# Kernel optimization log

Hardware: AMD Instinct MI355X
Metric: run time of the kernel (lower is better)

## Reference

```python
import jax, jax.numpy as jnp
import numpy as np

B, C, P, H, W, S = 4, 256, 128, 56, 56, 5
EPS = 1e-5


def setup_inputs() -> dict:
    key = jax.random.key(0)
    ks = jax.random.split(key, 6)
    return {
        "x": jax.random.normal(ks[0], (B, C, H, W), jnp.float32),
        "Wt": jax.random.normal(ks[1], (P, C), jnp.float32) * 0.05,
        "Wp": jax.random.normal(ks[2], (P, C), jnp.float32) * 0.05,
        "Wg": jax.random.normal(ks[3], (S, P, C), jnp.float32) * 0.05,
        "W1": jax.random.normal(ks[4], (S, C, P), jnp.float32) * 0.05,
        "W2": jax.random.normal(ks[5], (S, C, P), jnp.float32) * 0.05,
        "gamma": jnp.ones((S, C), jnp.float32),
        "beta": jnp.zeros((S, C), jnp.float32),
    }


def _batchnorm(o, g, b):
    # training-mode BN over (batch, spatial); o: [b, C, n]
    mean = o.mean(axis=(0, 2), keepdims=True)
    var = ((o - mean) ** 2).mean(axis=(0, 2), keepdims=True)
    return (o - mean) * jax.lax.rsqrt(var + EPS) * g[None, :, None] + b[None, :, None]


def reference(x, Wt, Wp, Wg, W1, W2, gamma, beta):
    b, c, h, w = x.shape
    n = h * w
    xf = x.reshape(b, c, n)
    # 1x1 conv projections == channel matmuls
    t = jax.nn.relu(jnp.einsum('pc,bcn->bpn', Wt, xf))  # is_norm branch uses relu
    p = jax.nn.relu(jnp.einsum('pc,bcn->bpn', Wp, xf))
    att = jnp.einsum('bpi,bpj->bij', t, p)              # [b, n, n] affinity
    att = 0.5 * (att + jnp.swapaxes(att, 1, 2))         # is_sys symmetrization
    d = att.sum(axis=2)                                  # degree [b, n]
    d_safe = jnp.where(d != 0, d, 1.0)
    d_inv = jnp.where(d != 0, jax.lax.rsqrt(d_safe), 0.0)
    att = att * d_inv[:, None, :] * d_inv[:, :, None]    # D^-1/2 A D^-1/2
    out = xf
    for s in range(S):  # fixed small stage count
        g = jnp.einsum('pc,bcn->bpn', Wg[s], out)        # [b, P, n]
        ag = jnp.einsum('bij,bpj->bpi', att, g)          # att @ g over spatial
        o = jnp.einsum('cp,bpn->bcn', W1[s], ag) + jnp.einsum('cp,bpn->bcn', W2[s], g)
        out = _batchnorm(o, gamma[s], beta[s]) + out     # BN + residual
    return out.reshape(b, c, h, w)
```

## Files before the change

### kernel.cpp

```cpp
#include <hip/hip_runtime.h>

namespace {

constexpr int Bc = 4;
constexpr int Cc = 256;
constexpr int Pc = 128;
constexpr int Nc = 3136;
constexpr int Sc = 5;
constexpr int KSn = 7;
constexpr int KCH = 448;
constexpr float EPSc = 1e-5f;

typedef __attribute__((ext_vector_type(8))) short bf16x8;
typedef __attribute__((ext_vector_type(4))) float f32x4;
typedef __attribute__((ext_vector_type(8))) unsigned short u16x8;
typedef __attribute__((ext_vector_type(4))) unsigned short u16x4;

__device__ inline float bf2f(unsigned short u) {
    return __uint_as_float(((unsigned)u) << 16);
}
__device__ inline unsigned short f2bf(float f) {
    unsigned u = __float_as_uint(f);
    return (unsigned short)((u + 0x7FFFu + ((u >> 16) & 1u)) >> 16);
}

template <int EPI, bool DUAL, int CMOUT, bool SPLITK, int BNSTAT, bool F32OUT>
__global__ __launch_bounds__(256) void mgemm(
    const unsigned short* __restrict__ A, int lda, long aB,
    const unsigned short* __restrict__ Bw, int ldb, long bB,
    const unsigned short* __restrict__ A2, const unsigned short* __restrict__ B2,
    unsigned short* __restrict__ outSM, int ldsm, long smB, long smSlice,
    unsigned short* __restrict__ outCM, long cmB,
    float* __restrict__ ps, float* __restrict__ ps2,
    int K, int kchunk, const float* __restrict__ dinv)
{
    constexpr int TB = 64 * 64 * 2;
    constexpr int NT = DUAL ? 4 : 2;
    __shared__ __align__(16) char lds[2 * NT * TB];

    int b, kstart, kend;
    long smOff;
    if (SPLITK) {
        b = blockIdx.z & 3;
        int ks = blockIdx.z >> 2;
        kstart = ks * kchunk;
        kend = kstart + kchunk;
        smOff = (long)ks * smSlice;
    } else {
        b = blockIdx.z; kstart = 0; kend = K; smOff = 0;
    }
    const int n0 = blockIdx.x * 64;
    const int m0 = blockIdx.y * 64;
    const int tid = threadIdx.x;
    const int w = tid >> 6, l = tid & 63;

    const unsigned short* Ab  = A + (size_t)b * aB + (size_t)m0 * lda;
    const unsigned short* A2b = DUAL ? (A2 + (size_t)b * aB + (size_t)m0 * lda) : nullptr;
    const unsigned short* Bb  = Bw + (size_t)b * bB + (size_t)n0 * ldb;
    const unsigned short* B2b = DUAL ? (B2 + (size_t)b * bB + (size_t)n0 * ldb) : nullptr;

    const int srow = w * 16 + (l >> 3);
    const int gsw = ((l & 7) ^ (l >> 3)) * 8;
    const size_t aO0 = (size_t)srow * lda + gsw;
    const size_t aO1 = aO0 + (size_t)8 * lda;
    const size_t bO0 = (size_t)srow * ldb + gsw;
    const size_t bO1 = bO0 + (size_t)8 * ldb;
    const int wch = w * 2048;

    f32x4 acc[4] = {};

    auto stage = [&](int buf, int k0) {
        char* base = lds + buf * (NT * TB);
        __builtin_amdgcn_global_load_lds(
            (const __attribute__((address_space(1))) void*)(Ab + k0 + aO0),
            (__attribute__((address_space(3))) void*)(base + wch), 16, 0, 0);
        __builtin_amdgcn_global_load_lds(
            (const __attribute__((address_space(1))) void*)(Ab + k0 + aO1),
            (__attribute__((address_space(3))) void*)(base + wch + 1024), 16, 0, 0);
        __builtin_amdgcn_global_load_lds(
            (const __attribute__((address_space(1))) void*)(Bb + k0 + bO0),
            (__attribute__((address_space(3))) void*)(base + TB + wch), 16, 0, 0);
        __builtin_amdgcn_global_load_lds(
            (const __attribute__((address_space(1))) void*)(Bb + k0 + bO1),
            (__attribute__((address_space(3))) void*)(base + TB + wch + 1024), 16, 0, 0);
        if (DUAL) {
            __builtin_amdgcn_global_load_lds(
                (const __attribute__((address_space(1))) void*)(A2b + k0 + aO0),
                (__attribute__((address_space(3))) void*)(base + 2 * TB + wch), 16, 0, 0);
            __builtin_amdgcn_global_load_lds(
                (const __attribute__((address_space(1))) void*)(A2b + k0 + aO1),
                (__attribute__((address_space(3))) void*)(base + 2 * TB + wch + 1024), 16, 0, 0);
            __builtin_amdgcn_global_load_lds(
                (const __attribute__((address_space(1))) void*)(B2b + k0 + bO0),
                (__attribute__((address_space(3))) void*)(base + 3 * TB + wch), 16, 0, 0);
            __builtin_amdgcn_global_load_lds(
                (const __attribute__((address_space(1))) void*)(B2b + k0 + bO1),
                (__attribute__((address_space(3))) void*)(base + 3 * TB + wch + 1024), 16, 0, 0);
        }
    };

    auto compute = [&](int buf) {
        const char* base = lds + buf * (NT * TB);
        const int lo = l & 15, gq = l >> 4;
        const int brow = w * 16 + lo;
#pragma unroll
        for (int kh = 0; kh < 2; ++kh) {
            const int lg = kh * 4 + gq;
            bf16x8 bf = *(const bf16x8*)(base + TB + brow * 128 + ((lg ^ (brow & 7)) << 4));
#pragma unroll
            for (int r = 0; r < 4; ++r) {
                int row = r * 16 + lo;
                bf16x8 af = *(const bf16x8*)(base + row * 128 + ((lg ^ (row & 7)) << 4));
                acc[r] = __builtin_amdgcn_mfma_f32_16x16x32_bf16(af, bf, acc[r], 0, 0, 0);
            }
            if (DUAL) {
                bf16x8 bf2 = *(const bf16x8*)(base + 3 * TB + brow * 128 + ((lg ^ (brow & 7)) << 4));
#pragma unroll
                for (int r = 0; r < 4; ++r) {
                    int row = r * 16 + lo;
                    bf16x8 a2 = *(const bf16x8*)(base + 2 * TB + row * 128 + ((lg ^ (row & 7)) << 4));
                    acc[r] = __builtin_amdgcn_mfma_f32_16x16x32_bf16(a2, bf2, acc[r], 0, 0, 0);
                }
            }
        }
    };

    stage(0, kstart);
    __syncthreads();
    const int nst = (kend - kstart) >> 6;
    for (int s = 0; s < nst; ++s) {
        if (s + 1 < nst) stage((s + 1) & 1, kstart + ((s + 1) << 6));
        compute(s & 1);
        __syncthreads();
    }

    float* ot = (float*)lds;
#pragma unroll
    for (int r = 0; r < 4; ++r) {
#pragma unroll
        for (int j = 0; j < 4; ++j) {
            float v = acc[r][j];
            if (EPI == 1) v = fmaxf(v, 0.f);
            ot[(r * 16 + (l >> 4) * 4 + j) * 65 + (w * 16 + (l & 15))] = v;
        }
    }
    __syncthreads();

    if (F32OUT) {
        const int r = tid >> 2, c0 = (tid & 3) * 16;
        float* dst = (float*)outSM + (size_t)b * smB + smOff +
                     (size_t)(m0 + r) * ldsm + n0 + c0;
#pragma unroll
        for (int k = 0; k < 4; ++k) {
            float4 v;
            v.x = ot[r * 65 + c0 + 4 * k + 0];
            v.y = ot[r * 65 + c0 + 4 * k + 1];
            v.z = ot[r * 65 + c0 + 4 * k + 2];
            v.w = ot[r * 65 + c0 + 4 * k + 3];
            *(float4*)(dst + 4 * k) = v;
        }
    } else {
        const int r = tid >> 2, c0 = (tid & 3) * 16;
        float sc = 1.f;
        if (EPI == 2) sc = 0.5f * dinv[(size_t)b * Nc + m0 + r];
        u16x8 o1, o2;
#pragma unroll
        for (int j = 0; j < 8; ++j) {
            float v = ot[r * 65 + c0 + j];
            if (EPI == 2) v *= sc;
            o1[j] = f2bf(v);
        }
#pragma unroll
        for (int j = 0; j < 8; ++j) {
            float v = ot[r * 65 + c0 + 8 + j];
            if (EPI == 2) v *= sc;
            o2[j] = f2bf(v);
        }
        unsigned short* dst = outSM + (size_t)b * smB + smOff +
                              (size_t)(m0 + r) * ldsm + n0 + c0;
        *(u16x8*)dst = o1;
        *(u16x8*)(dst + 8) = o2;
    }

    if (CMOUT) {
        const int c = tid >> 2, r0 = (tid & 3) * 16;
        const float* dv = dinv + (size_t)b * Nc + m0 + r0;
        u16x8 o1, o2;
#pragma unroll
        for (int j = 0; j < 8; ++j) {
            float v = ot[(r0 + j) * 65 + c];
            if (CMOUT == 2) v *= dv[j];
            o1[j] = f2bf(v);
        }
#pragma unroll
        for (int j = 0; j < 8; ++j) {
            float v = ot[(r0 + 8 + j) * 65 + c];
            if (CMOUT == 2) v *= dv[8 + j];
            o2[j] = f2bf(v);
        }
        unsigned short* dst = outCM + (size_t)b * cmB + (size_t)(n0 + c) * Nc + m0 + r0;
        *(u16x8*)dst = o1;
        *(u16x8*)(dst + 8) = o2;
    }

    if (BNSTAT) {
        float* p1 = (float*)(lds + 16896);
        float* p2 = p1 + 256;
        const int col = tid & 63, rq = tid >> 6;
        float s = 0.f, s2 = 0.f;
#pragma unroll
        for (int i = 0; i < 16; ++i) {
            float v = ot[(rq * 16 + i) * 65 + col];
            s += v;
            if (BNSTAT == 2) s2 = fmaf(v, v, s2);
        }
        p1[rq * 64 + col] = s;
        if (BNSTAT == 2) p2[rq * 64 + col] = s2;
        __syncthreads();
        if (tid < 64) {
            float a = 0.f, a2 = 0.f;
#pragma unroll
            for (int q = 0; q < 4; ++q) {
                a += p1[q * 64 + tid];
                if (BNSTAT == 2) a2 += p2[q * 64 + tid];
            }
            size_t slot = ((size_t)b * 49 + blockIdx.y) * 256 + n0 + tid;
            ps[slot] = a;
            if (BNSTAT == 2) ps2[slot] = a2;
        }
    }
}

__global__ __launch_bounds__(256) void cvtw_k(
    const float* __restrict__ Wt, const float* __restrict__ Wp,
    const float* __restrict__ Wg, const float* __restrict__ W1,
    const float* __restrict__ W2,
    unsigned short* __restrict__ Wcomb, unsigned short* __restrict__ Wgh,
    unsigned short* __restrict__ W1h, unsigned short* __restrict__ W2h)
{
    size_t e = ((size_t)blockIdx.x * 256 + threadIdx.x) * 4;
    const float* src; unsigned short* dst;
    if (e < 32768)            { src = Wt + e;                    dst = Wcomb + e; }
    else if (e < 65536)       { src = Wp + (e - 32768);          dst = Wcomb + e; }
    else if (e < 65536 + 163840)     { size_t o = e - 65536;          src = Wg + o; dst = Wgh + o; }
    else if (e < 65536 + 2 * 163840) { size_t o = e - 65536 - 163840; src = W1 + o; dst = W1h + o; }
    else                             { size_t o = e - 65536 - 327680; src = W2 + o; dst = W2h + o; }
    float4 v = *(const float4*)src;
    u16x4 t;
    t[0] = f2bf(v.x); t[1] = f2bf(v.y); t[2] = f2bf(v.z); t[3] = f2bf(v.w);
    *(u16x4*)dst = t;
}

__global__ __launch_bounds__(256) void xpin_k(
    const float* __restrict__ x, float* __restrict__ out_sm,
    unsigned short* __restrict__ outh)
{
    __shared__ float tb[64][65];
    int b = blockIdx.z, c0 = blockIdx.y * 64, n0 = blockIdx.x * 64;
    int t = threadIdx.x;
    {
        int ci = t >> 2, nb = (t & 3) * 16;
        const float* src = x + ((size_t)b * Cc + c0 + ci) * Nc + n0 + nb;
#pragma unroll
        for (int k = 0; k < 4; ++k) {
            float4 v = *(const float4*)(src + 4 * k);
            tb[ci][nb + 4 * k + 0] = v.x; tb[ci][nb + 4 * k + 1] = v.y;
            tb[ci][nb + 4 * k + 2] = v.z; tb[ci][nb + 4 * k + 3] = v.w;
        }
    }
    __syncthreads();
    {
        int r = t >> 2, cb = (t & 3) * 16;
        size_t off = ((size_t)b * Nc + n0 + r) * Cc + c0 + cb;
        float vv[16];
#pragma unroll
        for (int j = 0; j < 16; ++j) vv[j] = tb[cb + j][r];
        float* dst = out_sm + off;
#pragma unroll
        for (int k = 0; k < 4; ++k) {
            float4 v; v.x = vv[4*k]; v.y = vv[4*k+1]; v.z = vv[4*k+2]; v.w = vv[4*k+3];
            *(float4*)(dst + 4 * k) = v;
        }
        u16x8 h1, h2;
#pragma unroll
        for (int j = 0; j < 8; ++j) { h1[j] = f2bf(vv[j]); h2[j] = f2bf(vv[8 + j]); }
        unsigned short* dh = outh + off;
        *(u16x8*)dh = h1;
        *(u16x8*)(dh + 8) = h2;
    }
}

__global__ __launch_bounds__(256) void xpout_k(
    const float* __restrict__ out_sm, float* __restrict__ outp)
{
    __shared__ float tb[64][65];
    int b = blockIdx.z, c0 = blockIdx.y * 64, n0 = blockIdx.x * 64;
    int t = threadIdx.x;
    {
        int r = t >> 2, cb = (t & 3) * 16;
        const float* src = out_sm + ((size_t)b * Nc + n0 + r) * Cc + c0 + cb;
#pragma unroll
        for (int k = 0; k < 4; ++k) {
            float4 v = *(const float4*)(src + 4 * k);
            tb[r][cb + 4 * k + 0] = v.x; tb[r][cb + 4 * k + 1] = v.y;
            tb[r][cb + 4 * k + 2] = v.z; tb[r][cb + 4 * k + 3] = v.w;
        }
    }
    __syncthreads();
    {
        int c = t >> 2, rb = (t & 3) * 16;
        float vv[16];
#pragma unroll
        for (int j = 0; j < 16; ++j) vv[j] = tb[rb + j][c];
        float* dst = outp + ((size_t)b * Cc + c0 + c) * Nc + n0 + rb;
#pragma unroll
        for (int k = 0; k < 4; ++k) {
            float4 v; v.x = vv[4*k]; v.y = vv[4*k+1]; v.z = vv[4*k+2]; v.w = vv[4*k+3];
            *(float4*)(dst + 4 * k) = v;
        }
    }
}

__global__ __launch_bounds__(256) void dinv_k(
    const unsigned short* __restrict__ U, const float* __restrict__ rp,
    float* __restrict__ dinv)
{
    __shared__ float rsl[256];
    int b = blockIdx.y, tid = threadIdx.x;
    float s = 0.f;
    for (int j = 0; j < 49; ++j) s += rp[((size_t)b * 49 + j) * 256 + tid];
    rsl[tid ^ 128] = s;
    __syncthreads();
    int i = blockIdx.x * 256 + tid;
    if (i < Nc) {
        const unsigned short* row = U + ((size_t)b * Nc + i) * 256;
        float acc = 0.f;
        for (int q0 = 0; q0 < 256; q0 += 8) {
            u16x8 v = *(const u16x8*)(row + q0);
#pragma unroll
            for (int j = 0; j < 8; ++j) acc = fmaf(bf2f(v[j]), rsl[q0 + j], acc);
        }
        float d = 0.5f * acc;
        dinv[(size_t)b * Nc + i] = d > 0.f ? rsqrtf(d) : 0.f;
    }
}

__global__ __launch_bounds__(256) void redmst_k(
    const float* __restrict__ Cpart, unsigned short* __restrict__ MstT)
{
    int e8 = blockIdx.x * 256 + threadIdx.x;
    int bp = e8 >> 5, qc = e8 & 31;
    size_t dstOff = ((size_t)bp * 32 + qc) * 8;
    size_t srcOff = ((size_t)bp * 32 + (qc ^ 16)) * 8;
    float4 s0 = {0.f, 0.f, 0.f, 0.f}, s1 = {0.f, 0.f, 0.f, 0.f};
    for (int ks = 0; ks < KSn; ++ks) {
        const float* base = Cpart + (size_t)ks * (Bc * Pc * Cc) + srcOff;
        float4 v0 = *(const float4*)base;
        float4 v1 = *(const float4*)(base + 4);
        s0.x += v0.x; s0.y += v0.y; s0.z += v0.z; s0.w += v0.w;
        s1.x += v1.x; s1.y += v1.y; s1.z += v1.z; s1.w += v1.w;
    }
    u16x8 o;
    o[0] = f2bf(s0.x); o[1] = f2bf(s0.y); o[2] = f2bf(s0.z); o[3] = f2bf(s0.w);
    o[4] = f2bf(s1.x); o[5] = f2bf(s1.y); o[6] = f2bf(s1.z); o[7] = f2bf(s1.w);
    *(u16x8*)(MstT + dstOff) = o;
}

__global__ __launch_bounds__(256) void bnfin_k(
    const float* __restrict__ ps, const float* __restrict__ ps2,
    const float* __restrict__ gamma, const float* __restrict__ beta,
    float* __restrict__ scale, float* __restrict__ shift)
{
    int c = threadIdx.x;
    float a = 0.f, a2 = 0.f;
    for (int g = 0; g < 196; ++g) {
        a += ps[(size_t)g * 256 + c];
        a2 += ps2[(size_t)g * 256 + c];
    }
    const float inv = 1.f / (float)(Bc * Nc);
    float mean = a * inv;
    float var = a2 * inv - mean * mean;
    float sc = gamma[c] * rsqrtf(var + EPSc);
    scale[c] = sc;
    shift[c] = beta[c] - mean * sc;
}

__global__ __launch_bounds__(256) void bnapp_k(
    const unsigned short* __restrict__ o, const float* __restrict__ scale,
    const float* __restrict__ shift, float* __restrict__ out_sm,
    unsigned short* __restrict__ outh)
{
    __shared__ float lsc[256], lsh[256];
    int t = threadIdx.x;
    lsc[t] = scale[t];
    lsh[t] = shift[t];
    __syncthreads();
    size_t e = ((size_t)blockIdx.x * 256 + t) * 8;
    int c8 = (int)(e & 255);
    u16x8 ov = *(const u16x8*)(o + e);
    float* op = out_sm + e;
    float4 o1 = *(float4*)op, o2 = *(float4*)(op + 4);
    float r[8];
#pragma unroll
    for (int j = 0; j < 8; ++j) r[j] = fmaf(bf2f(ov[j]), lsc[c8 + j], lsh[c8 + j]);
    o1.x += r[0]; o1.y += r[1]; o1.z += r[2]; o1.w += r[3];
    o2.x += r[4]; o2.y += r[5]; o2.z += r[6]; o2.w += r[7];
    *(float4*)op = o1;
    *(float4*)(op + 4) = o2;
    u16x8 hv;
    hv[0] = f2bf(o1.x); hv[1] = f2bf(o1.y); hv[2] = f2bf(o1.z); hv[3] = f2bf(o1.w);
    hv[4] = f2bf(o2.x); hv[5] = f2bf(o2.y); hv[6] = f2bf(o2.z); hv[7] = f2bf(o2.w);
    *(u16x8*)(outh + e) = hv;
}

}

extern "C" void kernel_launch(void* const* d_in, const int* in_sizes, int n_in,
                              void* d_out, int out_size, void* d_ws, size_t ws_size,
                              hipStream_t stream) {
    const float* x     = (const float*)d_in[0];
    const float* Wt    = (const float*)d_in[1];
    const float* Wp    = (const float*)d_in[2];
    const float* Wg    = (const float*)d_in[3];
    const float* W1    = (const float*)d_in[4];
    const float* W2    = (const float*)d_in[5];
    const float* gamma = (const float*)d_in[6];
    const float* beta  = (const float*)d_in[7];

    char* p = (char*)d_ws;
    auto alloc = [&](size_t bytes) { char* r = p; p += (bytes + 255) & ~(size_t)255; return r; };
    float*          out_sm = (float*)         alloc((size_t)Bc * Nc * Cc * 4);
    unsigned short* outh   = (unsigned short*)alloc((size_t)Bc * Nc * Cc * 2);
    unsigned short* U_sm   = (unsigned short*)alloc((size_t)Bc * Nc * 256 * 2);
    unsigned short* U_cm   = (unsigned short*)alloc((size_t)Bc * 256 * Nc * 2);
    unsigned short* g_sm   = (unsigned short*)alloc((size_t)Bc * Nc * Pc * 2);
    unsigned short* g_cmd  = (unsigned short*)alloc((size_t)Bc * Pc * Nc * 2);
    unsigned short* ag_sm  = (unsigned short*)alloc((size_t)Bc * Nc * Pc * 2);
    unsigned short* o_sm   = (unsigned short*)alloc((size_t)Bc * Nc * Cc * 2);
    float*          Cpart  = (float*)         alloc((size_t)KSn * Bc * Pc * Cc * 4);
    unsigned short* MstT   = (unsigned short*)alloc((size_t)Bc * Pc * Cc * 2);
    unsigned short* Wcomb  = (unsigned short*)alloc((size_t)Cc * Cc * 2);
    unsigned short* Wgh    = (unsigned short*)alloc((size_t)Sc * Pc * Cc * 2);
    unsigned short* W1h    = (unsigned short*)alloc((size_t)Sc * Cc * Pc * 2);
    unsigned short* W2h    = (unsigned short*)alloc((size_t)Sc * Cc * Pc * 2);
    float*          rp     = (float*)         alloc((size_t)Bc * 49 * 256 * 4);
    float*          dinv   = (float*)         alloc((size_t)Bc * Nc * 4);
    float*          ps     = (float*)         alloc((size_t)196 * 256 * 4);
    float*          ps2    = (float*)         alloc((size_t)196 * 256 * 4);
    float*          scale  = (float*)         alloc(256 * 4);
    float*          shiftb = (float*)         alloc(256 * 4);

    const long NC256 = (long)Nc * 256;
    const long NC128 = (long)Nc * 128;
    dim3 blk(256);

    cvtw_k<<<544, blk, 0, stream>>>(Wt, Wp, Wg, W1, W2, Wcomb, Wgh, W1h, W2h);
    xpin_k<<<dim3(49, 4, Bc), blk, 0, stream>>>(x, out_sm, outh);

    mgemm<1, false, 1, false, 1, false><<<dim3(4, 49, Bc), blk, 0, stream>>>(
        outh, 256, NC256, Wcomb, 256, 0, nullptr, nullptr,
        U_sm, 256, NC256, 0, U_cm, (long)256 * Nc, rp, nullptr, 256, 0, nullptr);

    dinv_k<<<dim3(13, Bc), blk, 0, stream>>>(U_sm, rp, dinv);

    for (int s = 0; s < Sc; ++s) {
        mgemm<0, false, 2, false, 0, false><<<dim3(2, 49, Bc), blk, 0, stream>>>(
            outh, 256, NC256, Wgh + (size_t)s * Pc * Cc, 256, 0, nullptr, nullptr,
            g_sm, 128, NC128, 0, g_cmd, (long)Pc * Nc, nullptr, nullptr, 256, 0, dinv);
        mgemm<0, false, 0, true, 0, true><<<dim3(4, 2, KSn * Bc), blk, 0, stream>>>(
            g_cmd, Nc, (long)Pc * Nc, U_cm, Nc, (long)256 * Nc, nullptr, nullptr,
            (unsigned short*)Cpart, 256, (long)Pc * Cc, (long)Bc * Pc * Cc,
            nullptr, 0, nullptr, nullptr, Nc, KCH, nullptr);
        redmst_k<<<64, blk, 0, stream>>>(Cpart, MstT);
        mgemm<2, false, 0, false, 0, false><<<dim3(2, 49, Bc), blk, 0, stream>>>(
            U_sm, 256, NC256, MstT, 256, (long)Pc * Cc, nullptr, nullptr,
            ag_sm, 128, NC128, 0, nullptr, 0, nullptr, nullptr, 256, 0, dinv);
        mgemm<0, true, 0, false, 2, false><<<dim3(4, 49, Bc), blk, 0, stream>>>(
            ag_sm, 128, NC128, W1h + (size_t)s * Cc * Pc, 128, 0,
            g_sm, W2h + (size_t)s * Cc * Pc,
            o_sm, 256, NC256, 0, nullptr, 0, ps, ps2, 128, 0, nullptr);
        bnfin_k<<<1, blk, 0, stream>>>(ps, ps2, gamma + s * Cc, beta + s * Cc,
                                       scale, shiftb);
        bnapp_k<<<1568, blk, 0, stream>>>(o_sm, scale, shiftb, out_sm, outh);
    }

    xpout_k<<<dim3(49, 4, Bc), blk, 0, stream>>>(out_sm, (float*)d_out);
}
```

Baseline: 300.7 us.

## Widen GEMM tiles to 64x128, concatenate W1/W2 into one K=256 GEMM, parallelize bnfin

The shared GEMM kernel's output tile grows from 64x64 to 64x128, with each wave computing two 16-column MFMA blocks so every A fragment feeds two MFMAs. The DUAL path is dropped: g and ag are written into one interleaved [N,256] buffer and W1/W2 are packed into a concatenated weight, so the output projection becomes a single K=256 GEMM. The BN finalize kernel now spreads across 16 blocks with an LDS reduction instead of running as a single block. The aim is more operand reuse per LDS load and less launch and serial overhead. The cost is about half as many blocks for the already small grids, which lowers occupancy and parallelism, plus a larger LDS footprint.

After: 280.0 us. -6.9%, faster.

```diff
diff --git a/kernel.cpp b/kernel.cpp
--- a/kernel.cpp
+++ b/kernel.cpp
@@ -24,19 +24,19 @@
     return (unsigned short)((u + 0x7FFFu + ((u >> 16) & 1u)) >> 16);
 }
 
-template <int EPI, bool DUAL, int CMOUT, bool SPLITK, int BNSTAT, bool F32OUT>
+template <int EPI, int CMOUT, bool SPLITK, int BNSTAT, bool F32OUT>
 __global__ __launch_bounds__(256) void mgemm(
     const unsigned short* __restrict__ A, int lda, long aB,
     const unsigned short* __restrict__ Bw, int ldb, long bB,
-    const unsigned short* __restrict__ A2, const unsigned short* __restrict__ B2,
     unsigned short* __restrict__ outSM, int ldsm, long smB, long smSlice,
     unsigned short* __restrict__ outCM, long cmB,
     float* __restrict__ ps, float* __restrict__ ps2,
     int K, int kchunk, const float* __restrict__ dinv)
 {
-    constexpr int TB = 64 * 64 * 2;
-    constexpr int NT = DUAL ? 4 : 2;
-    __shared__ __align__(16) char lds[2 * NT * TB];
+    constexpr int TBA = 64 * 64 * 2;
+    constexpr int TBB = 128 * 64 * 2;
+    constexpr int BUF = TBA + TBB;
+    __shared__ __align__(16) char lds[2 * BUF];
 
     int b, kstart, kend;
     long smOff;
@@ -49,78 +49,57 @@
     } else {
         b = blockIdx.z; kstart = 0; kend = K; smOff = 0;
     }
-    const int n0 = blockIdx.x * 64;
+    const int n0 = blockIdx.x * 128;
     const int m0 = blockIdx.y * 64;
     const int tid = threadIdx.x;
     const int w = tid >> 6, l = tid & 63;
 
-    const unsigned short* Ab  = A + (size_t)b * aB + (size_t)m0 * lda;
-    const unsigned short* A2b = DUAL ? (A2 + (size_t)b * aB + (size_t)m0 * lda) : nullptr;
-    const unsigned short* Bb  = Bw + (size_t)b * bB + (size_t)n0 * ldb;
-    const unsigned short* B2b = DUAL ? (B2 + (size_t)b * bB + (size_t)n0 * ldb) : nullptr;
-
-    const int srow = w * 16 + (l >> 3);
+    const unsigned short* Ab = A + (size_t)b * aB + (size_t)m0 * lda;
+    const unsigned short* Bb = Bw + (size_t)b * bB + (size_t)n0 * ldb;
+
+    const int srow = w * 8 + (l >> 3);
     const int gsw = ((l & 7) ^ (l >> 3)) * 8;
-    const size_t aO0 = (size_t)srow * lda + gsw;
-    const size_t aO1 = aO0 + (size_t)8 * lda;
-    const size_t bO0 = (size_t)srow * ldb + gsw;
-    const size_t bO1 = bO0 + (size_t)8 * ldb;
-    const int wch = w * 2048;
-
-    f32x4 acc[4] = {};
+
+    f32x4 acc[4][2] = {};
 
     auto stage = [&](int buf, int k0) {
-        char* base = lds + buf * (NT * TB);
-        __builtin_amdgcn_global_load_lds(
-            (const __attribute__((address_space(1))) void*)(Ab + k0 + aO0),
-            (__attribute__((address_space(3))) void*)(base + wch), 16, 0, 0);
-        __builtin_amdgcn_global_load_lds(
-            (const __attribute__((address_space(1))) void*)(Ab + k0 + aO1),
-            (__attribute__((address_space(3))) void*)(base + wch + 1024), 16, 0, 0);
-        __builtin_amdgcn_global_load_lds(
-            (const __attribute__((address_space(1))) void*)(Bb + k0 + bO0),
-            (__attribute__((address_space(3))) void*)(base + TB + wch), 16, 0, 0);
-        __builtin_amdgcn_global_load_lds(
-            (const __attribute__((address_space(1))) void*)(Bb + k0 + bO1),
-            (__attribute__((address_space(3))) void*)(base + TB + wch + 1024), 16, 0, 0);
-        if (DUAL) {
+        char* base = lds + buf * BUF;
+#pragma unroll
+        for (int j = 0; j < 2; ++j) {
             __builtin_amdgcn_global_load_lds(
-                (const __attribute__((address_space(1))) void*)(A2b + k0 + aO0),
-                (__attribute__((address_space(3))) void*)(base + 2 * TB + wch), 16, 0, 0);
+                (const __attribute__((address_space(1))) void*)
+                    (Ab + (size_t)(j * 32 + srow) * lda + k0 + gsw),
+                (__attribute__((address_space(3))) void*)(base + j * 4096 + w * 1024),
+                16, 0, 0);
+        }
+#pragma unroll
+        for (int j = 0; j < 4; ++j) {
             __builtin_amdgcn_global_load_lds(
-                (const __attribute__((address_space(1))) void*)(A2b + k0 + aO1),
-                (__attribute__((address_space(3))) void*)(base + 2 * TB + wch + 1024), 16, 0, 0);
-            __builtin_amdgcn_global_load_lds(
-                (const __attribute__((address_space(1))) void*)(B2b + k0 + bO0),
-                (__attribute__((address_space(3))) void*)(base + 3 * TB + wch), 16, 0, 0);
-            __builtin_amdgcn_global_load_lds(
-                (const __attribute__((address_space(1))) void*)(B2b + k0 + bO1),
-                (__attribute__((address_space(3))) void*)(base + 3 * TB + wch + 1024), 16, 0, 0);
+                (const __attribute__((address_space(1))) void*)
+                    (Bb + (size_t)(j * 32 + srow) * ldb + k0 + gsw),
+                (__attribute__((address_space(3))) void*)(base + TBA + j * 4096 + w * 1024),
+                16, 0, 0);
         }
     };
 
     auto compute = [&](int buf) {
-        const char* base = lds + buf * (NT * TB);
+        const char* base = lds + buf * BUF;
         const int lo = l & 15, gq = l >> 4;
-        const int brow = w * 16 + lo;
 #pragma unroll
         for (int kh = 0; kh < 2; ++kh) {
             const int lg = kh * 4 + gq;
-            bf16x8 bf = *(const bf16x8*)(base + TB + brow * 128 + ((lg ^ (brow & 7)) << 4));
+            bf16x8 bf[2];
+#pragma unroll
+            for (int c = 0; c < 2; ++c) {
+                int brow = w * 32 + c * 16 + lo;
+                bf[c] = *(const bf16x8*)(base + TBA + brow * 128 + ((lg ^ (brow & 7)) << 4));
+            }
 #pragma unroll
             for (int r = 0; r < 4; ++r) {
                 int row = r * 16 + lo;
                 bf16x8 af = *(const bf16x8*)(base + row * 128 + ((lg ^ (row & 7)) << 4));
-                acc[r] = __builtin_amdgcn_mfma_f32_16x16x32_bf16(af, bf, acc[r], 0, 0, 0);
-            }
-            if (DUAL) {
-                bf16x8 bf2 = *(const bf16x8*)(base + 3 * TB + brow * 128 + ((lg ^ (brow & 7)) << 4));
-#pragma unroll
-                for (int r = 0; r < 4; ++r) {
-                    int row = r * 16 + lo;
-                    bf16x8 a2 = *(const bf16x8*)(base + 2 * TB + row * 128 + ((lg ^ (row & 7)) << 4));
-                    acc[r] = __builtin_amdgcn_mfma_f32_16x16x32_bf16(a2, bf2, acc[r], 0, 0, 0);
-                }
+                acc[r][0] = __builtin_amdgcn_mfma_f32_16x16x32_bf16(af, bf[0], acc[r][0], 0, 0, 0);
+                acc[r][1] = __builtin_amdgcn_mfma_f32_16x16x32_bf16(af, bf[1], acc[r][1], 0, 0, 0);
             }
         }
     };
@@ -135,98 +114,90 @@
     }
 
     float* ot = (float*)lds;
-#pragma unroll
-    for (int r = 0; r < 4; ++r) {
-#pragma unroll
-        for (int j = 0; j < 4; ++j) {
-            float v = acc[r][j];
-            if (EPI == 1) v = fmaxf(v, 0.f);
-            ot[(r * 16 + (l >> 4) * 4 + j) * 65 + (w * 16 + (l & 15))] = v;
-        }
-    }
-    __syncthreads();
-
-    if (F32OUT) {
-        const int r = tid >> 2, c0 = (tid & 3) * 16;
-        float* dst = (float*)outSM + (size_t)b * smB + smOff +
-                     (size_t)(m0 + r) * ldsm + n0 + c0;
+    {
+        const int lo = l & 15, gq = l >> 4;
+#pragma unroll
+        for (int r = 0; r < 4; ++r)
+#pragma unroll
+            for (int c = 0; c < 2; ++c)
+#pragma unroll
+                for (int j = 0; j < 4; ++j) {
+                    float v = acc[r][c][j];
+                    if (EPI == 1) v = fmaxf(v, 0.f);
+                    ot[(r * 16 + gq * 4 + j) * 132 + w * 32 + c * 16 + lo] = v;
+                }
+    }
+    __syncthreads();
+
+    {
+        const int r = tid >> 2, c0 = (tid & 3) * 32;
+        if (F32OUT) {
+            float* dst = (float*)outSM + (size_t)b * smB + smOff +
+                         (size_t)(m0 + r) * ldsm + n0 + c0;
+#pragma unroll
+            for (int k = 0; k < 8; ++k) {
+                float4 v;
+                v.x = ot[r * 132 + c0 + 4 * k + 0];
+                v.y = ot[r * 132 + c0 + 4 * k + 1];
+                v.z = ot[r * 132 + c0 + 4 * k + 2];
+                v.w = ot[r * 132 + c0 + 4 * k + 3];
+                *(float4*)(dst + 4 * k) = v;
+            }
+        } else {
+            float sc = 1.f;
+            if (EPI == 2) sc = 0.5f * dinv[(size_t)b * Nc + m0 + r];
+            unsigned short* dst = outSM + (size_t)b * smB + smOff +
+                                  (size_t)(m0 + r) * ldsm + n0 + c0;
+#pragma unroll
+            for (int k = 0; k < 4; ++k) {
+                u16x8 o;
+#pragma unroll
+                for (int j = 0; j < 8; ++j) {
+                    float v = ot[r * 132 + c0 + 8 * k + j];
+                    if (EPI == 2) v *= sc;
+                    o[j] = f2bf(v);
+                }
+                *(u16x8*)(dst + 8 * k) = o;
+            }
+        }
+    }
+
+    if (CMOUT) {
+        const int c = tid >> 1, r0 = (tid & 1) * 32;
+        const float* dv = dinv + (size_t)b * Nc + m0 + r0;
+        unsigned short* dst = outCM + (size_t)b * cmB + (size_t)(n0 + c) * Nc + m0 + r0;
 #pragma unroll
         for (int k = 0; k < 4; ++k) {
-            float4 v;
-            v.x = ot[r * 65 + c0 + 4 * k + 0];
-            v.y = ot[r * 65 + c0 + 4 * k + 1];
-            v.z = ot[r * 65 + c0 + 4 * k + 2];
-            v.w = ot[r * 65 + c0 + 4 * k + 3];
-            *(float4*)(dst + 4 * k) = v;
-        }
-    } else {
-        const int r = tid >> 2, c0 = (tid & 3) * 16;
-        float sc = 1.f;
-        if (EPI == 2) sc = 0.5f * dinv[(size_t)b * Nc + m0 + r];
-        u16x8 o1, o2;
-#pragma unroll
-        for (int j = 0; j < 8; ++j) {
-            float v = ot[r * 65 + c0 + j];
-            if (EPI == 2) v *= sc;
-            o1[j] = f2bf(v);
-        }
-#pragma unroll
-        for (int j = 0; j < 8; ++j) {
-            float v = ot[r * 65 + c0 + 8 + j];
-            if (EPI == 2) v *= sc;
-            o2[j] = f2bf(v);
-        }
-        unsigned short* dst = outSM + (size_t)b * smB + smOff +
-                              (size_t)(m0 + r) * ldsm + n0 + c0;
-        *(u16x8*)dst = o1;
-        *(u16x8*)(dst + 8) = o2;
-    }
-
-    if (CMOUT) {
-        const int c = tid >> 2, r0 = (tid & 3) * 16;
-        const float* dv = dinv + (size_t)b * Nc + m0 + r0;
-        u16x8 o1, o2;
-#pragma unroll
-        for (int j = 0; j < 8; ++j) {
-            float v = ot[(r0 + j) * 65 + c];
-            if (CMOUT == 2) v *= dv[j];
-            o1[j] = f2bf(v);
-        }
-#pragma unroll
-        for (int j = 0; j < 8; ++j) {
-            float v = ot[(r0 + 8 + j) * 65 + c];
-            if (CMOUT == 2) v *= dv[8 + j];
-            o2[j] = f2bf(v);
-        }
-        unsigned short* dst = outCM + (size_t)b * cmB + (size_t)(n0 + c) * Nc + m0 + r0;
-        *(u16x8*)dst = o1;
-        *(u16x8*)(dst + 8) = o2;
+            u16x8 o;
+#pragma unroll
+            for (int j = 0; j < 8; ++j) {
+                float v = ot[(r0 + 8 * k + j) * 132 + c];
+                if (CMOUT == 2) v *= dv[8 * k + j];
+                o[j] = f2bf(v);
+            }
+            *(u16x8*)(dst + 8 * k) = o;
+        }
     }
 
     if (BNSTAT) {
-        float* p1 = (float*)(lds + 16896);
+        float* p1 = (float*)(lds + 35840);
         float* p2 = p1 + 256;
-        const int col = tid & 63, rq = tid >> 6;
+        const int col = tid & 127, half = tid >> 7;
         float s = 0.f, s2 = 0.f;
 #pragma unroll
-        for (int i = 0; i < 16; ++i) {
-            float v = ot[(rq * 16 + i) * 65 + col];
+        for (int i = 0; i < 32; ++i) {
+            float v = ot[(half * 32 + i) * 132 + col];
             s += v;
             if (BNSTAT == 2) s2 = fmaf(v, v, s2);
         }
-        p1[rq * 64 + col] = s;
-        if (BNSTAT == 2) p2[rq * 64 + col] = s2;
+        p1[half * 128 + col] = s;
+        if (BNSTAT == 2) p2[half * 128 + col] = s2;
         __syncthreads();
-        if (tid < 64) {
-            float a = 0.f, a2 = 0.f;
-#pragma unroll
-            for (int q = 0; q < 4; ++q) {
-                a += p1[q * 64 + tid];
-                if (BNSTAT == 2) a2 += p2[q * 64 + tid];
-            }
+        if (tid < 128) {
+            float a = p1[tid] + p1[128 + tid];
             size_t slot = ((size_t)b * 49 + blockIdx.y) * 256 + n0 + tid;
             ps[slot] = a;
-            if (BNSTAT == 2) ps2[slot] = a2;
+            if (BNSTAT == 2) ps2[slot] = p2[tid] + p2[128 + tid];
         }
     }
 }
@@ -236,15 +207,21 @@
     const float* __restrict__ Wg, const float* __restrict__ W1,
     const float* __restrict__ W2,
     unsigned short* __restrict__ Wcomb, unsigned short* __restrict__ Wgh,
-    unsigned short* __restrict__ W1h, unsigned short* __restrict__ W2h)
+    unsigned short* __restrict__ Wcat)
 {
     size_t e = ((size_t)blockIdx.x * 256 + threadIdx.x) * 4;
     const float* src; unsigned short* dst;
-    if (e < 32768)            { src = Wt + e;                    dst = Wcomb + e; }
-    else if (e < 65536)       { src = Wp + (e - 32768);          dst = Wcomb + e; }
-    else if (e < 65536 + 163840)     { size_t o = e - 65536;          src = Wg + o; dst = Wgh + o; }
-    else if (e < 65536 + 2 * 163840) { size_t o = e - 65536 - 163840; src = W1 + o; dst = W1h + o; }
-    else                             { size_t o = e - 65536 - 327680; src = W2 + o; dst = W2h + o; }
+    if (e < 32768)      { src = Wt + e;           dst = Wcomb + e; }
+    else if (e < 65536) { src = Wp + (e - 32768); dst = Wcomb + e; }
+    else if (e < 65536 + 163840) {
+        size_t o = e - 65536; src = Wg + o; dst = Wgh + o;
+    } else if (e < 65536 + 2 * 163840) {
+        size_t o = e - 65536 - 163840; src = W1 + o;
+        dst = Wcat + ((o >> 7) << 8) + (o & 127);
+    } else {
+        size_t o = e - 65536 - 327680; src = W2 + o;
+        dst = Wcat + ((o >> 7) << 8) + 128 + (o & 127);
+    }
     float4 v = *(const float4*)src;
     u16x4 t;
     t[0] = f2bf(v.x); t[1] = f2bf(v.y); t[2] = f2bf(v.z); t[3] = f2bf(v.w);
@@ -371,18 +348,30 @@
     const float* __restrict__ gamma, const float* __restrict__ beta,
     float* __restrict__ scale, float* __restrict__ shift)
 {
-    int c = threadIdx.x;
+    __shared__ float l1[256], l2[256];
+    int t = threadIdx.x;
+    int c = blockIdx.x * 16 + (t & 15);
+    int gl = t >> 4;
     float a = 0.f, a2 = 0.f;
-    for (int g = 0; g < 196; ++g) {
+    for (int g = gl; g < 196; g += 16) {
         a += ps[(size_t)g * 256 + c];
         a2 += ps2[(size_t)g * 256 + c];
     }
-    const float inv = 1.f / (float)(Bc * Nc);
-    float mean = a * inv;
-    float var = a2 * inv - mean * mean;
-    float sc = gamma[c] * rsqrtf(var + EPSc);
-    scale[c] = sc;
-    shift[c] = beta[c] - mean * sc;
+    l1[t] = a; l2[t] = a2;
+    __syncthreads();
+    if (gl == 0) {
+#pragma unroll
+        for (int j = 1; j < 16; ++j) {
+            a += l1[j * 16 + (t & 15)];
+            a2 += l2[j * 16 + (t & 15)];
+        }
+        const float inv = 1.f / (float)(Bc * Nc);
+        float mean = a * inv;
+        float var = a2 * inv - mean * mean;
+        float sc = gamma[c] * rsqrtf(var + EPSc);
+        scale[c] = sc;
+        shift[c] = beta[c] - mean * sc;
+    }
 }
 
 __global__ __launch_bounds__(256) void bnapp_k(
@@ -433,16 +422,14 @@
     unsigned short* outh   = (unsigned short*)alloc((size_t)Bc * Nc * Cc * 2);
     unsigned short* U_sm   = (unsigned short*)alloc((size_t)Bc * Nc * 256 * 2);
     unsigned short* U_cm   = (unsigned short*)alloc((size_t)Bc * 256 * Nc * 2);
-    unsigned short* g_sm   = (unsigned short*)alloc((size_t)Bc * Nc * Pc * 2);
+    unsigned short* agg    = (unsigned short*)alloc((size_t)Bc * Nc * 256 * 2);
     unsigned short* g_cmd  = (unsigned short*)alloc((size_t)Bc * Pc * Nc * 2);
-    unsigned short* ag_sm  = (unsigned short*)alloc((size_t)Bc * Nc * Pc * 2);
     unsigned short* o_sm   = (unsigned short*)alloc((size_t)Bc * Nc * Cc * 2);
     float*          Cpart  = (float*)         alloc((size_t)KSn * Bc * Pc * Cc * 4);
     unsigned short* MstT   = (unsigned short*)alloc((size_t)Bc * Pc * Cc * 2);
     unsigned short* Wcomb  = (unsigned short*)alloc((size_t)Cc * Cc * 2);
     unsigned short* Wgh    = (unsigned short*)alloc((size_t)Sc * Pc * Cc * 2);
-    unsigned short* W1h    = (unsigned short*)alloc((size_t)Sc * Cc * Pc * 2);
-    unsigned short* W2h    = (unsigned short*)alloc((size_t)Sc * Cc * Pc * 2);
+    unsigned short* Wcat   = (unsigned short*)alloc((size_t)Sc * Cc * 256 * 2);
     float*          rp     = (float*)         alloc((size_t)Bc * 49 * 256 * 4);
     float*          dinv   = (float*)         alloc((size_t)Bc * Nc * 4);
     float*          ps     = (float*)         alloc((size_t)196 * 256 * 4);
@@ -451,36 +438,35 @@
     float*          shiftb = (float*)         alloc(256 * 4);
 
     const long NC256 = (long)Nc * 256;
-    const long NC128 = (long)Nc * 128;
     dim3 blk(256);
 
-    cvtw_k<<<544, blk, 0, stream>>>(Wt, Wp, Wg, W1, W2, Wcomb, Wgh, W1h, W2h);
+    cvtw_k<<<544, blk, 0, stream>>>(Wt, Wp, Wg, W1, W2, Wcomb, Wgh, Wcat);
     xpin_k<<<dim3(49, 4, Bc), blk, 0, stream>>>(x, out_sm, outh);
 
-    mgemm<1, false, 1, false, 1, false><<<dim3(4, 49, Bc), blk, 0, stream>>>(
-        outh, 256, NC256, Wcomb, 256, 0, nullptr, nullptr,
+    mgemm<1, 1, false, 1, false><<<dim3(2, 49, Bc), blk, 0, stream>>>(
+        outh, 256, NC256, Wcomb, 256, 0,
         U_sm, 256, NC256, 0, U_cm, (long)256 * Nc, rp, nullptr, 256, 0, nullptr);
 
     dinv_k<<<dim3(13, Bc), blk, 0, stream>>>(U_sm, rp, dinv);
 
     for (int s = 0; s < Sc; ++s) {
-        mgemm<0, false, 2, false, 0, false><<<dim3(2, 49, Bc), blk, 0, stream>>>(
-            outh, 256, NC256, Wgh + (size_t)s * Pc * Cc, 256, 0, nullptr, nullptr,
-            g_sm, 128, NC128, 0, g_cmd, (long)Pc * Nc, nullptr, nullptr, 256, 0, dinv);
-        mgemm<0, false, 0, true, 0, true><<<dim3(4, 2, KSn * Bc), blk, 0, stream>>>(
-            g_cmd, Nc, (long)Pc * Nc, U_cm, Nc, (long)256 * Nc, nullptr, nullptr,
+        mgemm<0, 2, false, 0, false><<<dim3(1, 49, Bc), blk, 0, stream>>>(
+            outh, 256, NC256, Wgh + (size_t)s * Pc * Cc, 256, 0,
+            agg + 128, 256, NC256, 0, g_cmd, (long)Pc * Nc, nullptr, nullptr,
+            256, 0, dinv);
+        mgemm<0, 0, true, 0, true><<<dim3(2, 2, KSn * Bc), blk, 0, stream>>>(
+            g_cmd, Nc, (long)Pc * Nc, U_cm, Nc, (long)256 * Nc,
             (unsigned short*)Cpart, 256, (long)Pc * Cc, (long)Bc * Pc * Cc,
             nullptr, 0, nullptr, nullptr, Nc, KCH, nullptr);
         redmst_k<<<64, blk, 0, stream>>>(Cpart, MstT);
-        mgemm<2, false, 0, false, 0, false><<<dim3(2, 49, Bc), blk, 0, stream>>>(
-            U_sm, 256, NC256, MstT, 256, (long)Pc * Cc, nullptr, nullptr,
-            ag_sm, 128, NC128, 0, nullptr, 0, nullptr, nullptr, 256, 0, dinv);
-        mgemm<0, true, 0, false, 2, false><<<dim3(4, 49, Bc), blk, 0, stream>>>(
-            ag_sm, 128, NC128, W1h + (size_t)s * Cc * Pc, 128, 0,
-            g_sm, W2h + (size_t)s * Cc * Pc,
-            o_sm, 256, NC256, 0, nullptr, 0, ps, ps2, 128, 0, nullptr);
-        bnfin_k<<<1, blk, 0, stream>>>(ps, ps2, gamma + s * Cc, beta + s * Cc,
-                                       scale, shiftb);
+        mgemm<2, 0, false, 0, false><<<dim3(1, 49, Bc), blk, 0, stream>>>(
+            U_sm, 256, NC256, MstT, 256, (long)Pc * Cc,
+            agg, 256, NC256, 0, nullptr, 0, nullptr, nullptr, 256, 0, dinv);
+        mgemm<0, 0, false, 2, false><<<dim3(2, 49, Bc), blk, 0, stream>>>(
+            agg, 256, NC256, Wcat + (size_t)s * Cc * 256, 256, 0,
+            o_sm, 256, NC256, 0, nullptr, 0, ps, ps2, 256, 0, nullptr);
+        bnfin_k<<<16, blk, 0, stream>>>(ps, ps2, gamma + s * Cc, beta + s * Cc,
+                                        scale, shiftb);
         bnapp_k<<<1568, blk, 0, stream>>>(o_sm, scale, shiftb, out_sm, outh);
     }
 
```
